# Optimization experiments

Hardware: AMD Instinct MI355X
Metric: run time of the kernel (lower is better)

## Reference

```python
import jax, jax.numpy as jnp
import numpy as np

EPS = 1e-5

def inorm(x, w, b):
    # InstanceNorm1d over token dim (axis=1), per (batch, feature); biased var
    m = x.mean(axis=1, keepdims=True)
    v = ((x - m) ** 2).mean(axis=1, keepdims=True)
    return (x - m) / jnp.sqrt(v + EPS) * w + b

def setup_inputs() -> dict:
    B, N, D, FH = 2, 512, 128, 512
    key = jax.random.key(0)
    ks = iter(jax.random.split(key, 48))
    rn = lambda shape, s=0.05: jax.random.normal(next(ks), shape, jnp.float32) * s
    inp = {
        'row_emb': jax.random.normal(next(ks), (B, N, D), jnp.float32),
        'col_emb': jax.random.normal(next(ks), (B, N, D), jnp.float32),
        'cost_mat': jax.random.uniform(next(ks), (B, N, N), jnp.float32),
        'coords': jax.random.uniform(next(ks), (B, N, 2), jnp.float32),
        'alpha': jnp.ones((1,), jnp.float32),
        # instance norm affine params (weight~1, bias~0)
        'n1_w': 1.0 + rn((D,)), 'n1_b': rn((D,)),
        'n2_w': 1.0 + rn((D,)), 'n2_b': rn((D,)),
        'n3_w': 1.0 + rn((D,)), 'n3_b': rn((D,)),
        'fn1_w': 1.0 + rn((D,)), 'fn1_b': rn((D,)),
        'fn2_w': 1.0 + rn((D,)), 'fn2_b': rn((D,)),
        # AFTFull projections (stored (in,out))
        'q_w': rn((D, D)), 'q_b': rn((D,)),
        'k_w': rn((D, D)), 'k_b': rn((D,)),
        'v_w': rn((D, D)), 'v_b': rn((D,)),
        'p_w': rn((D, D)), 'p_b': rn((D,)),
        'mhc_w': rn((D, D)), 'mhc_b': rn((D,)),
        # DistAngleFusion MLPs
        'dist_w1': rn((1, D)), 'dist_b1': rn((D,)),
        'dist_w2': rn((D, D)), 'dist_b2': rn((D,)),
        'ang_w1': rn((1, D)), 'ang_b1': rn((D,)),
        'ang_w2': rn((D, D)), 'ang_b2': rn((D,)),
        'gate_w': rn((2 * D, 1)), 'gate_b': rn((1,)),
        'outlin_w': rn((D, 1)), 'outlin_b': rn((1,)),
        # FeedForward
        'ffn_w1': rn((D, FH)), 'ffn_b1': rn((FH,)),
        'ffn_w2': rn((FH, D)), 'ffn_b2': rn((D,)),
    }
    return inp

def reference(row_emb, col_emb, cost_mat, coords, alpha,
              n1_w, n1_b, n2_w, n2_b, n3_w, n3_b, fn1_w, fn1_b, fn2_w, fn2_b,
              q_w, q_b, k_w, k_b, v_w, v_b, p_w, p_b, mhc_w, mhc_b,
              dist_w1, dist_b1, dist_w2, dist_b2,
              ang_w1, ang_b1, ang_w2, ang_b2,
              gate_w, gate_b, outlin_w, outlin_b,
              ffn_w1, ffn_b1, ffn_w2, ffn_b2):
    rn = inorm(row_emb, n1_w, n1_b)
    cn = inorm(col_emb, n2_w, n2_b)

    # DistAngleFusion: adapt_bias (B,N,N)
    diff = coords[:, :, None, :] - coords[:, None, :, :]  # (B,N,N,2)
    angles = jnp.arctan2(diff[..., 1], diff[..., 0])
    dist_e = jax.nn.relu(cost_mat[..., None] @ dist_w1 + dist_b1) @ dist_w2 + dist_b2  # (B,N,N,D)
    angle_e = jax.nn.relu(angles[..., None] @ ang_w1 + ang_b1) @ ang_w2 + ang_b2
    g = jax.nn.sigmoid(jnp.concatenate([dist_e, angle_e], axis=-1) @ gate_w + gate_b)  # (B,N,N,1)
    fused = g * dist_e + (1.0 - g) * angle_e
    adapt_bias = (fused @ outlin_w + outlin_b)[..., 0] * alpha  # (B,N,N)

    # AFTFull
    Q = jax.nn.sigmoid(rn @ q_w + q_b)          # (B,N,H)
    K = jax.nn.softmax(cn @ k_w + k_b, axis=1)  # softmax over tokens
    V = cn @ v_w + v_b
    eab = jnp.exp(jax.nn.softmax(adapt_bias, axis=-1))  # (B,N,N)
    eK = jnp.exp(K)
    num = jnp.einsum('bnm,bmh->bnh', eab, eK * V)
    den = jnp.einsum('bnm,bmh->bnh', eab, eK)
    Yt = (Q * (num / den)) @ p_w + p_b

    mh = inorm(Yt @ mhc_w + mhc_b, n3_w, n3_b)

    # TransformerFFN with instance norms
    x = inorm(rn + mh, fn1_w, fn1_b)
    ff = jax.nn.relu(x @ ffn_w1 + ffn_b1) @ ffn_w2 + ffn_b2
    return inorm(x + ff, fn2_w, fn2_b)
```

## Files before the change

kernel.cpp:

```cpp
#include <hip/hip_runtime.h>
#include <hip/hip_bf16.h>
#include <math.h>

#define Bn  2
#define Nn  512
#define Dn  128
#define FHn 512
#define BND (Bn*Nn*Dn)

typedef __hip_bfloat16 bf16;

__device__ __forceinline__ float cvt(float x) { return x; }
__device__ __forceinline__ float cvt(bf16 x) { return __bfloat162float(x); }
__device__ __forceinline__ float sigmoidf_(float x) { return 1.0f / (1.0f + expf(-x)); }
__device__ __forceinline__ bool is_bf16(const void* alpha) {
    return ((const unsigned short*)alpha)[0] == 0x3F80;
}

#define S_ 131072
#define WS_Q    (0 * S_)
#define WS_K    (1 * S_)
#define WS_V    (2 * S_)
#define WS_EK   (3 * S_)
#define WS_EKV  (4 * S_)
#define WS_EAB  (5 * S_)
#define WS_MH   (1 * S_)
#define WS_T    (2 * S_)
#define WS_OP   (3 * S_)
#define WS_ST   (9 * S_)

#define ST_IN_SC   0
#define ST_IN_SH   512
#define ST_X_SC    2048
#define ST_X_SH    2304
#define ST_PRE     3072
#define P_SC       1024
#define ST_TAB     4224

#define TAB_ANG 644
#define TAB_N   1288

#define SMEM_FLOATS 2568

struct KP {
    const void *row, *col, *cost, *coords, *alpha;
    const void *n1w, *n1b, *n2w, *n2b, *n3w, *n3b, *f1w, *f1b, *f2w, *f2b;
    const void *qw, *qb, *kw, *kb, *vw, *vb, *pw, *pb, *mw, *mb;
    const void *dw1, *db1, *dw2, *db2, *aw1, *ab1, *aw2, *ab2, *gw, *gb, *ow, *ob;
    const void *ffw1, *ffb1, *ffw2, *ffb2;
    void* out;
    float* ws;
};

__device__ __forceinline__ void blk_sum2(float& s, float& ss, volatile float* scr) {
#pragma unroll
    for (int off = 32; off > 0; off >>= 1) { s += __shfl_down(s, off); ss += __shfl_down(ss, off); }
    __syncthreads();
    int wave = threadIdx.x >> 6, lane = threadIdx.x & 63;
    if (lane == 0) { scr[wave] = s; scr[4 + wave] = ss; }
    __syncthreads();
    s = scr[0] + scr[1] + scr[2] + scr[3];
    ss = scr[4] + scr[5] + scr[6] + scr[7];
}

__device__ __forceinline__ float blk_sum1(float v, volatile float* scr) {
#pragma unroll
    for (int off = 32; off > 0; off >>= 1) v += __shfl_down(v, off);
    __syncthreads();
    int wave = threadIdx.x >> 6, lane = threadIdx.x & 63;
    if (lane == 0) scr[wave] = v;
    __syncthreads();
    return scr[0] + scr[1] + scr[2] + scr[3];
}

__device__ __forceinline__ float blk_max1(float v, volatile float* scr) {
#pragma unroll
    for (int off = 32; off > 0; off >>= 1) v = fmaxf(v, __shfl_down(v, off));
    __syncthreads();
    int wave = threadIdx.x >> 6, lane = threadIdx.x & 63;
    if (lane == 0) scr[wave] = v;
    __syncthreads();
    return fmaxf(fmaxf(scr[0], scr[1]), fmaxf(scr[2], scr[3]));
}

template <typename T>
__device__ void build_tables(const T* w1p, const T* b1p, const T* w2p,
                             const T* owp, const T* gwp, float* gtab, float* smem) {
    int tid = threadIdx.x;
    float* W  = smem;
    float* Bb = smem + 128;
    float* U  = smem + 256;
    float* Vv = smem + 384;
    float* Tt = smem + 512;
    int* RK   = (int*)(smem + 640);
    if (tid < 128) {
        float u = 0.f, v = 0.f;
#pragma unroll 4
        for (int d = 0; d < Dn; ++d) {
            float w2 = cvt(w2p[tid * Dn + d]);
            u += w2 * cvt(owp[d]);
            v += w2 * cvt(gwp[d]);
        }
        float w = cvt(w1p[tid]), b = cvt(b1p[tid]);
        U[tid] = u; Vv[tid] = v; W[tid] = w; Bb[tid] = b;
        Tt[tid] = (w != 0.f) ? (-b / w) : 3.0e38f;
    }
    __syncthreads();
    if (tid < 128) {
        float tk = Tt[tid]; int r = 0;
        for (int j = 0; j < 128; ++j) {
            float tj = Tt[j];
            r += (tj < tk) || (tj == tk && j < tid);
        }
        RK[tid] = r;
        gtab[r] = tk;
    }
    __syncthreads();
    if (tid <= 128) {
        int si = tid;
        float slS = 0, inS = 0, slT = 0, inT = 0;
        for (int k = 0; k < 128; ++k) {
            float w = W[k];
            if (w == 0.f) {
                float rb = fmaxf(Bb[k], 0.f);
                inS += rb * U[k];
                inT += rb * Vv[k];
            } else {
                bool act = (w > 0.f) ? (RK[k] < si) : (RK[k] >= si);
                if (act) {
                    slS += w * U[k];  inS += Bb[k] * U[k];
                    slT += w * Vv[k]; inT += Bb[k] * Vv[k];
                }
            }
        }
        gtab[128 + si] = slS;
        gtab[257 + si] = inS;
        gtab[386 + si] = slT;
        gtab[515 + si] = inT;
    }
}

__device__ __forceinline__ int bsearch128(const float* T, float c) {
    int lo = 0, hi = 128;
    while (lo < hi) { int mid = (lo + hi) >> 1; if (T[mid] <= c) lo = mid + 1; else hi = mid; }
    return lo;
}

template <typename T>
__device__ void phase0(const KP& p, float* st, float* smem) {
    float* scr = smem + 2560;
    int cid = blockIdx.x;
    int tid = threadIdx.x;
    {
        int which = cid >> 8, b = (cid >> 7) & 1, d = cid & 127;
        const T* src = (const T*)(which ? p.col : p.row) + (size_t)b * Nn * Dn + d;
        float x0 = cvt(src[(size_t)tid * Dn]);
        float x1 = cvt(src[(size_t)(tid + 256) * Dn]);
        float s = x0 + x1, ss = x0 * x0 + x1 * x1;
        blk_sum2(s, ss, scr);
        if (tid == 0) {
            float m = s * (1.f / Nn);
            float v = fmaxf(ss * (1.f / Nn) - m * m, 0.f);
            float rstd = rsqrtf(v + 1e-5f);
            const T* w = which ? (const T*)p.n2w : (const T*)p.n1w;
            const T* bb = which ? (const T*)p.n2b : (const T*)p.n1b;
            float sc = rstd * cvt(w[d]);
            st[ST_IN_SC + cid] = sc;
            st[ST_IN_SH + cid] = cvt(bb[d]) - m * sc;
        }
    }
    __syncthreads();
    if (cid == 128) {
        const T* db2 = (const T*)p.db2; const T* ab2 = (const T*)p.ab2;
        const T* ow = (const T*)p.ow;   const T* gw = (const T*)p.gw;
        float d2 = 0.f, a2 = 0.f, o = 0.f, g0 = 0.f, g1 = 0.f;
        if (tid < 128) {
            d2 = cvt(db2[tid]); a2 = cvt(ab2[tid]);
            o = cvt(ow[tid]); g0 = cvt(gw[tid]); g1 = cvt(gw[Dn + tid]);
        }
        float cds = d2 * o, cdt = d2 * g0, cas = a2 * o, cat = a2 * g1;
        blk_sum2(cds, cdt, scr);
        blk_sum2(cas, cat, scr);
        if (tid == 0) {
            float* pre = st + ST_PRE;
            pre[P_SC + 0] = cds; pre[P_SC + 1] = cdt;
            pre[P_SC + 2] = cas; pre[P_SC + 3] = cat;
            pre[P_SC + 4] = cvt(((const T*)p.gb)[0]);
            pre[P_SC + 5] = cvt(((const T*)p.ob)[0]);
            pre[P_SC + 6] = cvt(((const T*)p.alpha)[0]);
        }
    } else if (cid == 129) {
        build_tables<T>((const T*)p.dw1, (const T*)p.db1, (const T*)p.dw2,
                        (const T*)p.ow, (const T*)p.gw, st + ST_TAB, smem);
    } else if (cid == 130) {
        build_tables<T>((const T*)p.aw1, (const T*)p.ab1, (const T*)p.aw2,
                        (const T*)p.ow, (const T*)p.gw + Dn, st + ST_TAB + TAB_ANG, smem);
    }
}

template <typename T>
__device__ void phase1(const KP& p, float* st, float* smem) {
    int tid = threadIdx.x;
    int r0 = blockIdx.x * 2;
    int b = r0 >> 9;
    const T* row = (const T*)p.row; const T* col = (const T*)p.col;
    float* ws = p.ws;
    float* Q = ws + WS_Q; float* Kraw = ws + WS_K; float* V = ws + WS_V;

    float* lr = smem;
    float* lc = smem + 256;
    float* redq = smem + 512;
    float* redk = smem + 1024;
    float* redv = smem + 1536;
    {
        int r = tid >> 7, d = tid & 127;
        float scR = st[ST_IN_SC + b * 128 + d],       shR = st[ST_IN_SH + b * 128 + d];
        float scC = st[ST_IN_SC + 256 + b * 128 + d], shC = st[ST_IN_SH + 256 + b * 128 + d];
        lr[r * 128 + d] = cvt(row[(size_t)(r0 + r) * Dn + d]) * scR + shR;
        lc[r * 128 + d] = cvt(col[(size_t)(r0 + r) * Dn + d]) * scC + shC;
    }
    __syncthreads();
    {
        int h = tid & 127, half = tid >> 7;
        const T* qw = (const T*)p.qw; const T* kw = (const T*)p.kw; const T* vw = (const T*)p.vw;
        float q0 = 0, q1 = 0, ka = 0, kb_ = 0, v0 = 0, v1 = 0;
        int ks = half * 64;
#pragma unroll 8
        for (int k = ks; k < ks + 64; ++k) {
            float wq = cvt(qw[k * Dn + h]);
            float wk = cvt(kw[k * Dn + h]);
            float wv = cvt(vw[k * Dn + h]);
            q0 += lr[k] * wq;        q1 += lr[128 + k] * wq;
            ka += lc[k] * wk;        kb_ += lc[128 + k] * wk;
            v0 += lc[k] * wv;        v1 += lc[128 + k] * wv;
        }
        redq[half * 256 + h] = q0;  redq[half * 256 + 128 + h] = q1;
        redk[half * 256 + h] = ka;  redk[half * 256 + 128 + h] = kb_;
        redv[half * 256 + h] = v0;  redv[half * 256 + 128 + h] = v1;
    }
    __syncthreads();
    if (tid < 128) {
        int h = tid;
        float bq = cvt(((const T*)p.qb)[h]);
        float bk = cvt(((const T*)p.kb)[h]);
        float bv = cvt(((const T*)p.vb)[h]);
#pragma unroll
        for (int r = 0; r < 2; ++r) {
            Q[(r0 + r) * Dn + h]    = sigmoidf_(redq[r * 128 + h] + redq[256 + r * 128 + h] + bq);
            Kraw[(r0 + r) * Dn + h] = redk[r * 128 + h] + redk[256 + r * 128 + h] + bk;
            V[(r0 + r) * Dn + h]    = redv[r * 128 + h] + redv[256 + r * 128 + h] + bv;
        }
    }
    __syncthreads();

    float* abv = smem;
    float* red = smem + 512;
    float* tab = smem + 768;
    const float* gtab = st + ST_TAB;
    for (int e = tid; e < TAB_N; e += 256) tab[e] = gtab[e];
    __syncthreads();
    float* eab = ws + WS_EAB;
    const float* pre = st + ST_PRE;
    float cds = pre[P_SC + 0], cdt = pre[P_SC + 1], cas = pre[P_SC + 2], cat = pre[P_SC + 3];
    float gbias = pre[P_SC + 4], obias = pre[P_SC + 5], alpha = pre[P_SC + 6];
    const T* cost = (const T*)p.cost;
    const T* coords = (const T*)p.coords;

    for (int rr = 0; rr < 2; ++rr) {
        int rowi = r0 + rr;
        int bb_ = rowi >> 9, i = rowi & 511;
        float cix = cvt(coords[((size_t)bb_ * Nn + i) * 2 + 0]);
        float ciy = cvt(coords[((size_t)bb_ * Nn + i) * 2 + 1]);
        const T* crow = cost + (size_t)bb_ * Nn * Nn + (size_t)i * Nn;
#pragma unroll
        for (int jj = 0; jj < 2; ++jj) {
            int j = tid + jj * 256;
            float c = cvt(crow[j]);
            int si = bsearch128(tab, c);
            float sd = fmaf(tab[128 + si], c, tab[257 + si]) + cds;
            float td = fmaf(tab[386 + si], c, tab[515 + si]) + cdt;
            float dx = cix - cvt(coords[((size_t)bb_ * Nn + j) * 2 + 0]);
            float dy = ciy - cvt(coords[((size_t)bb_ * Nn + j) * 2 + 1]);
            float ang = (dx == 0.f && dy == 0.f) ? 0.f : atan2f(dy, dx);
            int ai = bsearch128(tab + TAB_ANG, ang);
            float sa = fmaf(tab[TAB_ANG + 128 + ai], ang, tab[TAB_ANG + 257 + ai]) + cas;
            float ta = fmaf(tab[TAB_ANG + 386 + ai], ang, tab[TAB_ANG + 515 + ai]) + cat;
            float gv = sigmoidf_(td + ta + gbias);
            abv[j] = alpha * (gv * sd + (1.f - gv) * sa + obias);
        }
        __syncthreads();
        float m = fmaxf(abv[tid], abv[tid + 256]);
        red[tid] = m; __syncthreads();
        for (int s = 128; s > 0; s >>= 1) {
            if (tid < s) red[tid] = fmaxf(red[tid], red[tid + s]);
            __syncthreads();
        }
        m = red[0];
        __syncthreads();
        float e0 = expf(abv[tid] - m), e1 = expf(abv[tid + 256] - m);
        red[tid] = e0 + e1; __syncthreads();
        for (int s = 128; s > 0; s >>= 1) {
            if (tid < s) red[tid] += red[tid + s];
            __syncthreads();
        }
        float rsum = 1.f / red[0];
        float* orow = eab + (size_t)rowi * Nn;
        orow[tid] = expf(e0 * rsum);
        orow[tid + 256] = expf(e1 * rsum);
        __syncthreads();
    }
}

__device__ void phase2(const KP& p, float* smem) {
    float* scr = smem + 2560;
    int tid = threadIdx.x;
    int c = blockIdx.x;
    int b = c >> 7, h = c & 127;
    float* ws = p.ws;
    const float* Kraw = ws + WS_K;
    const float* V = ws + WS_V;
    float* eK = ws + WS_EK;
    float* eKV = ws + WS_EKV;
    const float* kb = Kraw + (size_t)b * Nn * Dn + h;
    const float* vb = V + (size_t)b * Nn * Dn + h;
    float x0 = kb[(size_t)tid * Dn];
    float x1 = kb[(size_t)(tid + 256) * Dn];
    float mx = blk_max1(fmaxf(x0, x1), scr);
    float e0 = expf(x0 - mx), e1 = expf(x1 - mx);
    float s = blk_sum1(e0 + e1, scr);
    float rs = 1.f / s;
    size_t a0 = (size_t)b * Nn * Dn + (size_t)tid * Dn + h;
    size_t a1 = (size_t)b * Nn * Dn + (size_t)(tid + 256) * Dn + h;
    float ek0 = expf(e0 * rs), ek1 = expf(e1 * rs);
    eK[a0] = ek0;  eKV[a0] = ek0 * vb[(size_t)tid * Dn];
    eK[a1] = ek1;  eKV[a1] = ek1 * vb[(size_t)(tid + 256) * Dn];
}

template <typename T>
__device__ void phase3(const KP& p, float* smem) {
    int tid = threadIdx.x;
    int r0 = blockIdx.x * 4;
    int b = r0 >> 9;
    float* ws = p.ws;
    const float* eab = ws + WS_EAB;
    const float* eK = ws + WS_EK;
    const float* eKV = ws + WS_EKV;
    const float* Q = ws + WS_Q;
    float* mh = ws + WS_MH;

    float* ab   = smem;
    float* redn = smem + 2048;
    float* redd = smem + 4096;
    float* gl   = smem + 6144;
    float* yl   = smem + 6656;

    {
        float4* ab4 = (float4*)ab;
        const float4* g4 = (const float4*)(eab + (size_t)r0 * Nn);
        ab4[tid] = g4[tid];
    }
    __syncthreads();
    int h = tid & 127, q = tid >> 7;
    {
        float num[4] = {0,0,0,0}, den[4] = {0,0,0,0};
        int j0 = q * 128;
        const float* ekb = eK + (size_t)b * Nn * Dn + h;
        const float* evb = eKV + (size_t)b * Nn * Dn + h;
#pragma unroll 4
        for (int j = j0; j < j0 + 128; ++j) {
            float ek = ekb[(size_t)j * Dn];
            float ev = evb[(size_t)j * Dn];
#pragma unroll
            for (int r = 0; r < 4; ++r) {
                num[r] += ab[r * 512 + j] * ev;
                den[r] += ab[r * 512 + j] * ek;
            }
        }
#pragma unroll
        for (int r = 0; r < 4; ++r) {
            redn[q * 512 + r * 128 + h] = num[r];
            redd[q * 512 + r * 128 + h] = den[r];
        }
    }
    __syncthreads();
    if (tid < 128) {
#pragma unroll
        for (int r = 0; r < 4; ++r) {
            float nu = redn[r * 128 + h] + redn[512 + r * 128 + h]
                     + redn[1024 + r * 128 + h] + redn[1536 + r * 128 + h];
            float de = redd[r * 128 + h] + redd[512 + r * 128 + h]
                     + redd[1024 + r * 128 + h] + redd[1536 + r * 128 + h];
            gl[r * 128 + h] = Q[(r0 + r) * Dn + h] * nu / de;
        }
    }
    __syncthreads();
    {
        const T* pw = (const T*)p.pw;
        float acc[4] = {0,0,0,0};
        int ks = q * 32;
#pragma unroll 8
        for (int k = ks; k < ks + 32; ++k) {
            float w = cvt(pw[k * Dn + h]);
#pragma unroll
            for (int r = 0; r < 4; ++r) acc[r] += gl[r * 128 + k] * w;
        }
#pragma unroll
        for (int r = 0; r < 4; ++r) redn[q * 512 + r * 128 + h] = acc[r];
    }
    __syncthreads();
    if (tid < 128) {
        float bp = cvt(((const T*)p.pb)[h]);
#pragma unroll
        for (int r = 0; r < 4; ++r)
            yl[r * 128 + h] = redn[r * 128 + h] + redn[512 + r * 128 + h]
                            + redn[1024 + r * 128 + h] + redn[1536 + r * 128 + h] + bp;
    }
    __syncthreads();
    {
        const T* mw = (const T*)p.mw;
        float acc[4] = {0,0,0,0};
        int ks = q * 32;
#pragma unroll 8
        for (int k = ks; k < ks + 32; ++k) {
            float w = cvt(mw[k * Dn + h]);
#pragma unroll
            for (int r = 0; r < 4; ++r) acc[r] += yl[r * 128 + k] * w;
        }
#pragma unroll
        for (int r = 0; r < 4; ++r) redn[q * 512 + r * 128 + h] = acc[r];
    }
    __syncthreads();
    if (tid < 128) {
        float bm = cvt(((const T*)p.mb)[h]);
#pragma unroll
        for (int r = 0; r < 4; ++r)
            mh[(r0 + r) * Dn + h] = redn[r * 128 + h] + redn[512 + r * 128 + h]
                                  + redn[1024 + r * 128 + h] + redn[1536 + r * 128 + h] + bm;
    }
}

template <typename T>
__device__ void phase45(const KP& p, float* st, float* smem) {
    float* scr = smem + 2560;
    int tid = threadIdx.x;
    int c = blockIdx.x;
    int b = c >> 7, d = c & 127;
    const float* mh = p.ws + WS_MH;
    const float* mp = mh + (size_t)b * Nn * Dn + d;
    float m0 = mp[(size_t)tid * Dn], m1 = mp[(size_t)(tid + 256) * Dn];
    float s = m0 + m1, ss = m0 * m0 + m1 * m1;
    blk_sum2(s, ss, scr);
    float mm = s * (1.f / Nn);
    float vv = fmaxf(ss * (1.f / Nn) - mm * mm, 0.f);
    float rstd = rsqrtf(vv + 1e-5f);
    float scM = rstd * cvt(((const T*)p.n3w)[d]);
    float shM = cvt(((const T*)p.n3b)[d]) - mm * scM;
    const T* row = (const T*)p.row;
    float scI = st[ST_IN_SC + c], shI = st[ST_IN_SH + c];
    const T* rp = row + (size_t)b * Nn * Dn + d;
    float* tp = p.ws + WS_T + (size_t)b * Nn * Dn + d;
    float x0 = cvt(rp[(size_t)tid * Dn]) * scI + shI + m0 * scM + shM;
    float x1 = cvt(rp[(size_t)(tid + 256) * Dn]) * scI + shI + m1 * scM + shM;
    tp[(size_t)tid * Dn] = x0;
    tp[(size_t)(tid + 256) * Dn] = x1;
    __syncthreads();
    float s2 = x0 + x1, ss2 = x0 * x0 + x1 * x1;
    blk_sum2(s2, ss2, scr);
    if (tid == 0) {
        float m = s2 * (1.f / Nn);
        float v = fmaxf(ss2 * (1.f / Nn) - m * m, 0.f);
        float r = rsqrtf(v + 1e-5f);
        float sc = r * cvt(((const T*)p.f1w)[d]);
        st[ST_X_SC + c] = sc;
        st[ST_X_SH + c] = cvt(((const T*)p.f1b)[d]) - m * sc;
    }
}

template <typename T>
__device__ void phase6(const KP& p, float* st, float* smem) {
    int tid = threadIdx.x;
    int r0 = blockIdx.x * 4;
    int b = r0 >> 9;
    const float* t = p.ws + WS_T;
    float* outpre = p.ws + WS_OP;
    const T* w1 = (const T*)p.ffw1; const T* b1 = (const T*)p.ffb1;
    const T* w2 = (const T*)p.ffw2; const T* b2 = (const T*)p.ffb2;

    float* xl = smem;
    float* hl = smem + 512;
    float* red = smem + 2560;
    {
        int r = tid >> 7, d = tid & 127;
        int c = b * 128 + d;
        xl[r * 128 + d] = t[(r0 + r) * Dn + d] * st[ST_X_SC + c] + st[ST_X_SH + c];
    }
    __syncthreads();
    {
        int f = tid;
        float a[4] = {0,0,0,0};
#pragma unroll 4
        for (int k = 0; k < Dn; ++k) {
            float w = cvt(w1[k * FHn + f]);
#pragma unroll
            for (int r = 0; r < 4; ++r) a[r] += xl[r * 128 + k] * w;
        }
        float bb1 = cvt(b1[f]);
#pragma unroll
        for (int r = 0; r < 4; ++r) hl[r * 512 + f] = fmaxf(a[r] + bb1, 0.f);
    }
    __syncthreads();
    {
        int d = tid & 127, q = tid >> 7;
        int k0 = q * 128;
        float a[4] = {0,0,0,0};
#pragma unroll 8
        for (int k = k0; k < k0 + 128; ++k) {
            float w = cvt(w2[k * Dn + d]);
#pragma unroll
            for (int r = 0; r < 4; ++r) a[r] += hl[r * 512 + k] * w;
        }
#pragma unroll
        for (int r = 0; r < 4; ++r) red[q * 512 + r * 128 + d] = a[r];
    }
    __syncthreads();
    if (tid < 128) {
        float bb2 = cvt(b2[tid]);
#pragma unroll
        for (int r = 0; r < 4; ++r) {
            float sum = red[r * 128 + tid] + red[512 + r * 128 + tid]
                      + red[1024 + r * 128 + tid] + red[1536 + r * 128 + tid];
            outpre[(r0 + r) * Dn + tid] = xl[r * 128 + tid] + sum + bb2;
        }
    }
}

template <typename T>
__device__ void phase78(const KP& p, float* smem) {
    float* scr = smem + 2560;
    int tid = threadIdx.x;
    int c = blockIdx.x;
    int b = c >> 7, d = c & 127;
    const float* op = p.ws + WS_OP;
    const float* sp = op + (size_t)b * Nn * Dn + d;
    float x0 = sp[(size_t)tid * Dn], x1 = sp[(size_t)(tid + 256) * Dn];
    float s = x0 + x1, ss = x0 * x0 + x1 * x1;
    blk_sum2(s, ss, scr);
    float m = s * (1.f / Nn);
    float v = fmaxf(ss * (1.f / Nn) - m * m, 0.f);
    float rstd = rsqrtf(v + 1e-5f);
    float sc = rstd * cvt(((const T*)p.f2w)[d]);
    float sh = cvt(((const T*)p.f2b)[d]) - m * sc;
    T* out = (T*)p.out + (size_t)b * Nn * Dn + d;
    out[(size_t)tid * Dn] = (T)(x0 * sc + sh);
    out[(size_t)(tid + 256) * Dn] = (T)(x1 * sc + sh);
}

#define PH_WRAP(name, call_bf, call_f)                                        \
__global__ __launch_bounds__(256) void name(KP p) {                           \
    __shared__ float smem[SMEM_FLOATS];                                       \
    float* st = p.ws + WS_ST; (void)st;                                       \
    if (is_bf16(p.alpha)) { call_bf; } else { call_f; }                       \
}

PH_WRAP(k_head,  phase0<bf16>(p, st, smem),  phase0<float>(p, st, smem))
PH_WRAP(k_qkveab, phase1<bf16>(p, st, smem), phase1<float>(p, st, smem))
__global__ __launch_bounds__(256) void k_kekv(KP p) {
    __shared__ float smem[SMEM_FLOATS];
    phase2(p, smem);
}
__global__ __launch_bounds__(512) void k_attn(KP p) {
    __shared__ float smem[7168];
    if (is_bf16(p.alpha)) phase3<bf16>(p, smem);
    else                  phase3<float>(p, smem);
}
PH_WRAP(k_mid,   phase45<bf16>(p, st, smem), phase45<float>(p, st, smem))
__global__ __launch_bounds__(512) void k_ffn(KP p) {
    __shared__ float smem[4608];
    float* st = p.ws + WS_ST;
    if (is_bf16(p.alpha)) phase6<bf16>(p, st, smem);
    else                  phase6<float>(p, st, smem);
}
PH_WRAP(k_tail,  phase78<bf16>(p, smem),     phase78<float>(p, smem))

extern "C" void kernel_launch(void* const* d_in, const int* in_sizes, int n_in,
                              void* d_out, int out_size, void* d_ws, size_t ws_size,
                              hipStream_t stream) {
    KP p;
    p.row = d_in[0];  p.col = d_in[1];  p.cost = d_in[2];  p.coords = d_in[3];
    p.alpha = d_in[4];
    p.n1w = d_in[5];  p.n1b = d_in[6];  p.n2w = d_in[7];  p.n2b = d_in[8];
    p.n3w = d_in[9];  p.n3b = d_in[10]; p.f1w = d_in[11]; p.f1b = d_in[12];
    p.f2w = d_in[13]; p.f2b = d_in[14];
    p.qw = d_in[15];  p.qb = d_in[16];  p.kw = d_in[17];  p.kb = d_in[18];
    p.vw = d_in[19];  p.vb = d_in[20];  p.pw = d_in[21];  p.pb = d_in[22];
    p.mw = d_in[23];  p.mb = d_in[24];
    p.dw1 = d_in[25]; p.db1 = d_in[26]; p.dw2 = d_in[27]; p.db2 = d_in[28];
    p.aw1 = d_in[29]; p.ab1 = d_in[30]; p.aw2 = d_in[31]; p.ab2 = d_in[32];
    p.gw = d_in[33];  p.gb = d_in[34];  p.ow = d_in[35];  p.ob = d_in[36];
    p.ffw1 = d_in[37]; p.ffb1 = d_in[38]; p.ffw2 = d_in[39]; p.ffb2 = d_in[40];
    p.out = d_out;
    p.ws = (float*)d_ws;

    k_head<<<512, 256, 0, stream>>>(p);
    k_qkveab<<<512, 256, 0, stream>>>(p);
    k_kekv<<<256, 256, 0, stream>>>(p);
    k_attn<<<256, 512, 0, stream>>>(p);
    k_mid<<<256, 256, 0, stream>>>(p);
    k_ffn<<<256, 512, 0, stream>>>(p);
    k_tail<<<256, 256, 0, stream>>>(p);
}
```

Baseline: 240.8 us.

## Fuse seven phase kernels into one cooperative kernel with grid syncs

After: 435.6 us. 1.81x slower.

```diff
diff --git a/kernel.cpp b/kernel.cpp
--- a/kernel.cpp
+++ b/kernel.cpp
@@ -1,12 +1,14 @@
 #include <hip/hip_runtime.h>
 #include <hip/hip_bf16.h>
+#include <hip/hip_cooperative_groups.h>
 #include <math.h>
+
+namespace cg = cooperative_groups;
 
 #define Bn  2
 #define Nn  512
 #define Dn  128
 #define FHn 512
-#define BND (Bn*Nn*Dn)
 
 typedef __hip_bfloat16 bf16;
 
@@ -40,7 +42,7 @@
 #define TAB_ANG 644
 #define TAB_N   1288
 
-#define SMEM_FLOATS 2568
+#define SMEM_FLOATS 7232
 
 struct KP {
     const void *row, *col, *cost, *coords, *alpha;
@@ -52,35 +54,55 @@
     float* ws;
 };
 
-__device__ __forceinline__ void blk_sum2(float& s, float& ss, volatile float* scr) {
+__device__ __forceinline__ void blk512_sum2(float& s, float& ss, volatile float* scr) {
 #pragma unroll
     for (int off = 32; off > 0; off >>= 1) { s += __shfl_down(s, off); ss += __shfl_down(ss, off); }
     __syncthreads();
     int wave = threadIdx.x >> 6, lane = threadIdx.x & 63;
-    if (lane == 0) { scr[wave] = s; scr[4 + wave] = ss; }
-    __syncthreads();
-    s = scr[0] + scr[1] + scr[2] + scr[3];
-    ss = scr[4] + scr[5] + scr[6] + scr[7];
-}
-
-__device__ __forceinline__ float blk_sum1(float v, volatile float* scr) {
+    if (lane == 0) { scr[wave] = s; scr[8 + wave] = ss; }
+    __syncthreads();
+    s = 0.f; ss = 0.f;
+#pragma unroll
+    for (int w = 0; w < 8; ++w) { s += scr[w]; ss += scr[8 + w]; }
+}
+
+__device__ __forceinline__ float blk512_sum1(float v, volatile float* scr) {
 #pragma unroll
     for (int off = 32; off > 0; off >>= 1) v += __shfl_down(v, off);
     __syncthreads();
     int wave = threadIdx.x >> 6, lane = threadIdx.x & 63;
     if (lane == 0) scr[wave] = v;
     __syncthreads();
-    return scr[0] + scr[1] + scr[2] + scr[3];
-}
-
-__device__ __forceinline__ float blk_max1(float v, volatile float* scr) {
+    float s = 0.f;
+#pragma unroll
+    for (int w = 0; w < 8; ++w) s += scr[w];
+    return s;
+}
+
+__device__ __forceinline__ float blk512_max1(float v, volatile float* scr) {
 #pragma unroll
     for (int off = 32; off > 0; off >>= 1) v = fmaxf(v, __shfl_down(v, off));
     __syncthreads();
     int wave = threadIdx.x >> 6, lane = threadIdx.x & 63;
     if (lane == 0) scr[wave] = v;
     __syncthreads();
-    return fmaxf(fmaxf(scr[0], scr[1]), fmaxf(scr[2], scr[3]));
+    float m = scr[0];
+#pragma unroll
+    for (int w = 1; w < 8; ++w) m = fmaxf(m, scr[w]);
+    return m;
+}
+
+__device__ __forceinline__ void grp_sum2(float& s, float& ss, volatile float* scr) {
+#pragma unroll
+    for (int off = 32; off > 0; off >>= 1) { s += __shfl_down(s, off); ss += __shfl_down(ss, off); }
+    __syncthreads();
+    int tid = threadIdx.x;
+    int wave = tid >> 6, lane = tid & 63;
+    if (lane == 0) { scr[wave] = s; scr[8 + wave] = ss; }
+    __syncthreads();
+    int base = (tid >> 8) * 4;
+    s  = scr[base] + scr[base + 1] + scr[base + 2] + scr[base + 3];
+    ss = scr[8 + base] + scr[8 + base + 1] + scr[8 + base + 2] + scr[8 + base + 3];
 }
 
 template <typename T>
@@ -147,30 +169,32 @@
 }
 
 template <typename T>
-__device__ void phase0(const KP& p, float* st, float* smem) {
-    float* scr = smem + 2560;
-    int cid = blockIdx.x;
-    int tid = threadIdx.x;
-    {
-        int which = cid >> 8, b = (cid >> 7) & 1, d = cid & 127;
-        const T* src = (const T*)(which ? p.col : p.row) + (size_t)b * Nn * Dn + d;
-        float x0 = cvt(src[(size_t)tid * Dn]);
-        float x1 = cvt(src[(size_t)(tid + 256) * Dn]);
+__device__ void phase0_f(const KP& p, float* st, float* smem) {
+    float* scr = smem + 7168;
+    int tid = threadIdx.x;
+    int bid = blockIdx.x;
+    int g = tid >> 8, t = tid & 255;
+    int cid = bid + g * 256;
+    {
+        int b = (bid >> 7) & 1, d = bid & 127;
+        const T* src = (const T*)(g ? p.col : p.row) + (size_t)b * Nn * Dn + d;
+        float x0 = cvt(src[(size_t)t * Dn]);
+        float x1 = cvt(src[(size_t)(t + 256) * Dn]);
         float s = x0 + x1, ss = x0 * x0 + x1 * x1;
-        blk_sum2(s, ss, scr);
-        if (tid == 0) {
+        grp_sum2(s, ss, scr);
+        if (t == 0) {
             float m = s * (1.f / Nn);
             float v = fmaxf(ss * (1.f / Nn) - m * m, 0.f);
             float rstd = rsqrtf(v + 1e-5f);
-            const T* w = which ? (const T*)p.n2w : (const T*)p.n1w;
-            const T* bb = which ? (const T*)p.n2b : (const T*)p.n1b;
+            const T* w = g ? (const T*)p.n2w : (const T*)p.n1w;
+            const T* bb = g ? (const T*)p.n2b : (const T*)p.n1b;
             float sc = rstd * cvt(w[d]);
             st[ST_IN_SC + cid] = sc;
             st[ST_IN_SH + cid] = cvt(bb[d]) - m * sc;
         }
     }
     __syncthreads();
-    if (cid == 128) {
+    if (bid == 128) {
         const T* db2 = (const T*)p.db2; const T* ab2 = (const T*)p.ab2;
         const T* ow = (const T*)p.ow;   const T* gw = (const T*)p.gw;
         float d2 = 0.f, a2 = 0.f, o = 0.f, g0 = 0.f, g1 = 0.f;
@@ -179,8 +203,8 @@
             o = cvt(ow[tid]); g0 = cvt(gw[tid]); g1 = cvt(gw[Dn + tid]);
         }
         float cds = d2 * o, cdt = d2 * g0, cas = a2 * o, cat = a2 * g1;
-        blk_sum2(cds, cdt, scr);
-        blk_sum2(cas, cat, scr);
+        blk512_sum2(cds, cdt, scr);
+        blk512_sum2(cas, cat, scr);
         if (tid == 0) {
             float* pre = st + ST_PRE;
             pre[P_SC + 0] = cds; pre[P_SC + 1] = cdt;
@@ -189,29 +213,30 @@
             pre[P_SC + 5] = cvt(((const T*)p.ob)[0]);
             pre[P_SC + 6] = cvt(((const T*)p.alpha)[0]);
         }
-    } else if (cid == 129) {
+    } else if (bid == 129) {
         build_tables<T>((const T*)p.dw1, (const T*)p.db1, (const T*)p.dw2,
                         (const T*)p.ow, (const T*)p.gw, st + ST_TAB, smem);
-    } else if (cid == 130) {
+    } else if (bid == 130) {
         build_tables<T>((const T*)p.aw1, (const T*)p.ab1, (const T*)p.aw2,
                         (const T*)p.ow, (const T*)p.gw + Dn, st + ST_TAB + TAB_ANG, smem);
     }
 }
 
 template <typename T>
-__device__ void phase1(const KP& p, float* st, float* smem) {
-    int tid = threadIdx.x;
-    int r0 = blockIdx.x * 2;
+__device__ void phase1_f(const KP& p, float* st, float* smem) {
+    int tid = threadIdx.x;
+    int r0 = blockIdx.x * 4;
     int b = r0 >> 9;
     const T* row = (const T*)p.row; const T* col = (const T*)p.col;
     float* ws = p.ws;
     float* Q = ws + WS_Q; float* Kraw = ws + WS_K; float* V = ws + WS_V;
+    float* scr = smem + 7168;
 
     float* lr = smem;
-    float* lc = smem + 256;
-    float* redq = smem + 512;
-    float* redk = smem + 1024;
-    float* redv = smem + 1536;
+    float* lc = smem + 512;
+    float* redq = smem + 1024;
+    float* redk = smem + 3072;
+    float* redv = smem + 5120;
     {
         int r = tid >> 7, d = tid & 127;
         float scR = st[ST_IN_SC + b * 128 + d],       shR = st[ST_IN_SH + b * 128 + d];
@@ -221,22 +246,28 @@
     }
     __syncthreads();
     {
-        int h = tid & 127, half = tid >> 7;
+        int h = tid & 127, q = tid >> 7;
         const T* qw = (const T*)p.qw; const T* kw = (const T*)p.kw; const T* vw = (const T*)p.vw;
-        float q0 = 0, q1 = 0, ka = 0, kb_ = 0, v0 = 0, v1 = 0;
-        int ks = half * 64;
+        float aq[4] = {0,0,0,0}, ak[4] = {0,0,0,0}, av[4] = {0,0,0,0};
+        int ks = q * 32;
 #pragma unroll 8
-        for (int k = ks; k < ks + 64; ++k) {
+        for (int k = ks; k < ks + 32; ++k) {
             float wq = cvt(qw[k * Dn + h]);
             float wk = cvt(kw[k * Dn + h]);
             float wv = cvt(vw[k * Dn + h]);
-            q0 += lr[k] * wq;        q1 += lr[128 + k] * wq;
-            ka += lc[k] * wk;        kb_ += lc[128 + k] * wk;
-            v0 += lc[k] * wv;        v1 += lc[128 + k] * wv;
-        }
-        redq[half * 256 + h] = q0;  redq[half * 256 + 128 + h] = q1;
-        redk[half * 256 + h] = ka;  redk[half * 256 + 128 + h] = kb_;
-        redv[half * 256 + h] = v0;  redv[half * 256 + 128 + h] = v1;
+#pragma unroll
+            for (int r = 0; r < 4; ++r) {
+                aq[r] += lr[r * 128 + k] * wq;
+                ak[r] += lc[r * 128 + k] * wk;
+                av[r] += lc[r * 128 + k] * wv;
+            }
+        }
+#pragma unroll
+        for (int r = 0; r < 4; ++r) {
+            redq[q * 512 + r * 128 + h] = aq[r];
+            redk[q * 512 + r * 128 + h] = ak[r];
+            redv[q * 512 + r * 128 + h] = av[r];
+        }
     }
     __syncthreads();
     if (tid < 128) {
@@ -245,19 +276,20 @@
         float bk = cvt(((const T*)p.kb)[h]);
         float bv = cvt(((const T*)p.vb)[h]);
 #pragma unroll
-        for (int r = 0; r < 2; ++r) {
-            Q[(r0 + r) * Dn + h]    = sigmoidf_(redq[r * 128 + h] + redq[256 + r * 128 + h] + bq);
-            Kraw[(r0 + r) * Dn + h] = redk[r * 128 + h] + redk[256 + r * 128 + h] + bk;
-            V[(r0 + r) * Dn + h]    = redv[r * 128 + h] + redv[256 + r * 128 + h] + bv;
-        }
-    }
-    __syncthreads();
-
-    float* abv = smem;
-    float* red = smem + 512;
-    float* tab = smem + 768;
+        for (int r = 0; r < 4; ++r) {
+            float qv = redq[r*128+h] + redq[512 + r*128+h] + redq[1024 + r*128+h] + redq[1536 + r*128+h] + bq;
+            float kv = redk[r*128+h] + redk[512 + r*128+h] + redk[1024 + r*128+h] + redk[1536 + r*128+h] + bk;
+            float vv = redv[r*128+h] + redv[512 + r*128+h] + redv[1024 + r*128+h] + redv[1536 + r*128+h] + bv;
+            Q[(r0 + r) * Dn + h]    = sigmoidf_(qv);
+            Kraw[(r0 + r) * Dn + h] = kv;
+            V[(r0 + r) * Dn + h]    = vv;
+        }
+    }
+    __syncthreads();
+
+    float* tab = smem;
     const float* gtab = st + ST_TAB;
-    for (int e = tid; e < TAB_N; e += 256) tab[e] = gtab[e];
+    for (int e = tid; e < TAB_N; e += 512) tab[e] = gtab[e];
     __syncthreads();
     float* eab = ws + WS_EAB;
     const float* pre = st + ST_PRE;
@@ -266,53 +298,80 @@
     const T* cost = (const T*)p.cost;
     const T* coords = (const T*)p.coords;
 
-    for (int rr = 0; rr < 2; ++rr) {
+    int j = tid;
+    float aval[4];
+#pragma unroll
+    for (int rr = 0; rr < 4; ++rr) {
         int rowi = r0 + rr;
         int bb_ = rowi >> 9, i = rowi & 511;
         float cix = cvt(coords[((size_t)bb_ * Nn + i) * 2 + 0]);
         float ciy = cvt(coords[((size_t)bb_ * Nn + i) * 2 + 1]);
-        const T* crow = cost + (size_t)bb_ * Nn * Nn + (size_t)i * Nn;
-#pragma unroll
-        for (int jj = 0; jj < 2; ++jj) {
-            int j = tid + jj * 256;
-            float c = cvt(crow[j]);
-            int si = bsearch128(tab, c);
-            float sd = fmaf(tab[128 + si], c, tab[257 + si]) + cds;
-            float td = fmaf(tab[386 + si], c, tab[515 + si]) + cdt;
-            float dx = cix - cvt(coords[((size_t)bb_ * Nn + j) * 2 + 0]);
-            float dy = ciy - cvt(coords[((size_t)bb_ * Nn + j) * 2 + 1]);
-            float ang = (dx == 0.f && dy == 0.f) ? 0.f : atan2f(dy, dx);
-            int ai = bsearch128(tab + TAB_ANG, ang);
-            float sa = fmaf(tab[TAB_ANG + 128 + ai], ang, tab[TAB_ANG + 257 + ai]) + cas;
-            float ta = fmaf(tab[TAB_ANG + 386 + ai], ang, tab[TAB_ANG + 515 + ai]) + cat;
-            float gv = sigmoidf_(td + ta + gbias);
-            abv[j] = alpha * (gv * sd + (1.f - gv) * sa + obias);
+        float c = cvt(cost[(size_t)bb_ * Nn * Nn + (size_t)i * Nn + j]);
+        int si = bsearch128(tab, c);
+        float sd = fmaf(tab[128 + si], c, tab[257 + si]) + cds;
+        float td = fmaf(tab[386 + si], c, tab[515 + si]) + cdt;
+        float dx = cix - cvt(coords[((size_t)bb_ * Nn + j) * 2 + 0]);
+        float dy = ciy - cvt(coords[((size_t)bb_ * Nn + j) * 2 + 1]);
+        float ang = (dx == 0.f && dy == 0.f) ? 0.f : atan2f(dy, dx);
+        int ai = bsearch128(tab + TAB_ANG, ang);
+        float sa = fmaf(tab[TAB_ANG + 128 + ai], ang, tab[TAB_ANG + 257 + ai]) + cas;
+        float ta = fmaf(tab[TAB_ANG + 386 + ai], ang, tab[TAB_ANG + 515 + ai]) + cat;
+        float gv = sigmoidf_(td + ta + gbias);
+        aval[rr] = alpha * (gv * sd + (1.f - gv) * sa + obias);
+    }
+    int wave = tid >> 6, lane = tid & 63;
+    float mx[4];
+    {
+        float t0 = aval[0], t1 = aval[1], t2 = aval[2], t3 = aval[3];
+#pragma unroll
+        for (int off = 32; off > 0; off >>= 1) {
+            t0 = fmaxf(t0, __shfl_down(t0, off));
+            t1 = fmaxf(t1, __shfl_down(t1, off));
+            t2 = fmaxf(t2, __shfl_down(t2, off));
+            t3 = fmaxf(t3, __shfl_down(t3, off));
         }
         __syncthreads();
-        float m = fmaxf(abv[tid], abv[tid + 256]);
-        red[tid] = m; __syncthreads();
-        for (int s = 128; s > 0; s >>= 1) {
-            if (tid < s) red[tid] = fmaxf(red[tid], red[tid + s]);
-            __syncthreads();
-        }
-        m = red[0];
+        if (lane == 0) { scr[wave] = t0; scr[8 + wave] = t1; scr[16 + wave] = t2; scr[24 + wave] = t3; }
         __syncthreads();
-        float e0 = expf(abv[tid] - m), e1 = expf(abv[tid + 256] - m);
-        red[tid] = e0 + e1; __syncthreads();
-        for (int s = 128; s > 0; s >>= 1) {
-            if (tid < s) red[tid] += red[tid + s];
-            __syncthreads();
-        }
-        float rsum = 1.f / red[0];
-        float* orow = eab + (size_t)rowi * Nn;
-        orow[tid] = expf(e0 * rsum);
-        orow[tid + 256] = expf(e1 * rsum);
+#pragma unroll
+        for (int rr = 0; rr < 4; ++rr) {
+            float m = scr[rr * 8];
+#pragma unroll
+            for (int w = 1; w < 8; ++w) m = fmaxf(m, scr[rr * 8 + w]);
+            mx[rr] = m;
+        }
+    }
+    float ev[4];
+#pragma unroll
+    for (int rr = 0; rr < 4; ++rr) ev[rr] = expf(aval[rr] - mx[rr]);
+    float rs[4];
+    {
+        float t0 = ev[0], t1 = ev[1], t2 = ev[2], t3 = ev[3];
+#pragma unroll
+        for (int off = 32; off > 0; off >>= 1) {
+            t0 += __shfl_down(t0, off);
+            t1 += __shfl_down(t1, off);
+            t2 += __shfl_down(t2, off);
+            t3 += __shfl_down(t3, off);
+        }
         __syncthreads();
-    }
-}
-
-__device__ void phase2(const KP& p, float* smem) {
-    float* scr = smem + 2560;
+        if (lane == 0) { scr[wave] = t0; scr[8 + wave] = t1; scr[16 + wave] = t2; scr[24 + wave] = t3; }
+        __syncthreads();
+#pragma unroll
+        for (int rr = 0; rr < 4; ++rr) {
+            float s = 0.f;
+#pragma unroll
+            for (int w = 0; w < 8; ++w) s += scr[rr * 8 + w];
+            rs[rr] = 1.f / s;
+        }
+    }
+#pragma unroll
+    for (int rr = 0; rr < 4; ++rr)
+        eab[(size_t)(r0 + rr) * Nn + j] = expf(ev[rr] * rs[rr]);
+}
+
+__device__ void phase2_f(const KP& p, float* smem) {
+    float* scr = smem + 7168;
     int tid = threadIdx.x;
     int c = blockIdx.x;
     int b = c >> 7, h = c & 127;
@@ -324,20 +383,17 @@
     const float* kb = Kraw + (size_t)b * Nn * Dn + h;
     const float* vb = V + (size_t)b * Nn * Dn + h;
     float x0 = kb[(size_t)tid * Dn];
-    float x1 = kb[(size_t)(tid + 256) * Dn];
-    float mx = blk_max1(fmaxf(x0, x1), scr);
-    float e0 = expf(x0 - mx), e1 = expf(x1 - mx);
-    float s = blk_sum1(e0 + e1, scr);
-    float rs = 1.f / s;
+    float mx = blk512_max1(x0, scr);
+    float e0 = expf(x0 - mx);
+    float s = blk512_sum1(e0, scr);
+    float rsv = 1.f / s;
     size_t a0 = (size_t)b * Nn * Dn + (size_t)tid * Dn + h;
-    size_t a1 = (size_t)b * Nn * Dn + (size_t)(tid + 256) * Dn + h;
-    float ek0 = expf(e0 * rs), ek1 = expf(e1 * rs);
+    float ek0 = expf(e0 * rsv);
     eK[a0] = ek0;  eKV[a0] = ek0 * vb[(size_t)tid * Dn];
-    eK[a1] = ek1;  eKV[a1] = ek1 * vb[(size_t)(tid + 256) * Dn];
-}
-
-template <typename T>
-__device__ void phase3(const KP& p, float* smem) {
+}
+
+template <typename T>
+__device__ void phase3_f(const KP& p, float* smem) {
     int tid = threadIdx.x;
     int r0 = blockIdx.x * 4;
     int b = r0 >> 9;
@@ -367,13 +423,13 @@
         const float* ekb = eK + (size_t)b * Nn * Dn + h;
         const float* evb = eKV + (size_t)b * Nn * Dn + h;
 #pragma unroll 4
-        for (int j = j0; j < j0 + 128; ++j) {
-            float ek = ekb[(size_t)j * Dn];
-            float ev = evb[(size_t)j * Dn];
+        for (int jj = j0; jj < j0 + 128; ++jj) {
+            float ek = ekb[(size_t)jj * Dn];
+            float ev = evb[(size_t)jj * Dn];
 #pragma unroll
             for (int r = 0; r < 4; ++r) {
-                num[r] += ab[r * 512 + j] * ev;
-                den[r] += ab[r * 512 + j] * ek;
+                num[r] += ab[r * 512 + jj] * ev;
+                den[r] += ab[r * 512 + jj] * ek;
             }
         }
 #pragma unroll
@@ -440,16 +496,16 @@
 }
 
 template <typename T>
-__device__ void phase45(const KP& p, float* st, float* smem) {
-    float* scr = smem + 2560;
+__device__ void phase45_f(const KP& p, float* st, float* smem) {
+    float* scr = smem + 7168;
     int tid = threadIdx.x;
     int c = blockIdx.x;
     int b = c >> 7, d = c & 127;
     const float* mh = p.ws + WS_MH;
     const float* mp = mh + (size_t)b * Nn * Dn + d;
-    float m0 = mp[(size_t)tid * Dn], m1 = mp[(size_t)(tid + 256) * Dn];
-    float s = m0 + m1, ss = m0 * m0 + m1 * m1;
-    blk_sum2(s, ss, scr);
+    float m0 = mp[(size_t)tid * Dn];
+    float s = m0, ss = m0 * m0;
+    blk512_sum2(s, ss, scr);
     float mm = s * (1.f / Nn);
     float vv = fmaxf(ss * (1.f / Nn) - mm * mm, 0.f);
     float rstd = rsqrtf(vv + 1e-5f);
@@ -460,12 +516,9 @@
     const T* rp = row + (size_t)b * Nn * Dn + d;
     float* tp = p.ws + WS_T + (size_t)b * Nn * Dn + d;
     float x0 = cvt(rp[(size_t)tid * Dn]) * scI + shI + m0 * scM + shM;
-    float x1 = cvt(rp[(size_t)(tid + 256) * Dn]) * scI + shI + m1 * scM + shM;
     tp[(size_t)tid * Dn] = x0;
-    tp[(size_t)(tid + 256) * Dn] = x1;
-    __syncthreads();
-    float s2 = x0 + x1, ss2 = x0 * x0 + x1 * x1;
-    blk_sum2(s2, ss2, scr);
+    float s2 = x0, ss2 = x0 * x0;
+    blk512_sum2(s2, ss2, scr);
     if (tid == 0) {
         float m = s2 * (1.f / Nn);
         float v = fmaxf(ss2 * (1.f / Nn) - m * m, 0.f);
@@ -477,7 +530,7 @@
 }
 
 template <typename T>
-__device__ void phase6(const KP& p, float* st, float* smem) {
+__device__ void phase6_f(const KP& p, float* st, float* smem) {
     int tid = threadIdx.x;
     int r0 = blockIdx.x * 4;
     int b = r0 >> 9;
@@ -535,16 +588,16 @@
 }
 
 template <typename T>
-__device__ void phase78(const KP& p, float* smem) {
-    float* scr = smem + 2560;
+__device__ void phase78_f(const KP& p, float* smem) {
+    float* scr = smem + 7168;
     int tid = threadIdx.x;
     int c = blockIdx.x;
     int b = c >> 7, d = c & 127;
     const float* op = p.ws + WS_OP;
     const float* sp = op + (size_t)b * Nn * Dn + d;
-    float x0 = sp[(size_t)tid * Dn], x1 = sp[(size_t)(tid + 256) * Dn];
-    float s = x0 + x1, ss = x0 * x0 + x1 * x1;
-    blk_sum2(s, ss, scr);
+    float x0 = sp[(size_t)tid * Dn];
+    float s = x0, ss = x0 * x0;
+    blk512_sum2(s, ss, scr);
     float m = s * (1.f / Nn);
     float v = fmaxf(ss * (1.f / Nn) - m * m, 0.f);
     float rstd = rsqrtf(v + 1e-5f);
@@ -552,35 +605,32 @@
     float sh = cvt(((const T*)p.f2b)[d]) - m * sc;
     T* out = (T*)p.out + (size_t)b * Nn * Dn + d;
     out[(size_t)tid * Dn] = (T)(x0 * sc + sh);
-    out[(size_t)(tid + 256) * Dn] = (T)(x1 * sc + sh);
-}
-
-#define PH_WRAP(name, call_bf, call_f)                                        \
-__global__ __launch_bounds__(256) void name(KP p) {                           \
-    __shared__ float smem[SMEM_FLOATS];                                       \
-    float* st = p.ws + WS_ST; (void)st;                                       \
-    if (is_bf16(p.alpha)) { call_bf; } else { call_f; }                       \
-}
-
-PH_WRAP(k_head,  phase0<bf16>(p, st, smem),  phase0<float>(p, st, smem))
-PH_WRAP(k_qkveab, phase1<bf16>(p, st, smem), phase1<float>(p, st, smem))
-__global__ __launch_bounds__(256) void k_kekv(KP p) {
+}
+
+template <typename T>
+__device__ void run_all(const KP& p, float* smem, cg::grid_group& grid) {
+    float* st = p.ws + WS_ST;
+    phase0_f<T>(p, st, smem);
+    grid.sync();
+    phase1_f<T>(p, st, smem);
+    grid.sync();
+    phase2_f(p, smem);
+    grid.sync();
+    phase3_f<T>(p, smem);
+    grid.sync();
+    phase45_f<T>(p, st, smem);
+    grid.sync();
+    phase6_f<T>(p, st, smem);
+    grid.sync();
+    phase78_f<T>(p, smem);
+}
+
+__global__ __launch_bounds__(512, 1) void k_all(KP p) {
     __shared__ float smem[SMEM_FLOATS];
-    phase2(p, smem);
-}
-__global__ __launch_bounds__(512) void k_attn(KP p) {
-    __shared__ float smem[7168];
-    if (is_bf16(p.alpha)) phase3<bf16>(p, smem);
-    else                  phase3<float>(p, smem);
-}
-PH_WRAP(k_mid,   phase45<bf16>(p, st, smem), phase45<float>(p, st, smem))
-__global__ __launch_bounds__(512) void k_ffn(KP p) {
-    __shared__ float smem[4608];
-    float* st = p.ws + WS_ST;
-    if (is_bf16(p.alpha)) phase6<bf16>(p, st, smem);
-    else                  phase6<float>(p, st, smem);
-}
-PH_WRAP(k_tail,  phase78<bf16>(p, smem),     phase78<float>(p, smem))
+    cg::grid_group grid = cg::this_grid();
+    if (is_bf16(p.alpha)) run_all<bf16>(p, smem, grid);
+    else                  run_all<float>(p, smem, grid);
+}
 
 extern "C" void kernel_launch(void* const* d_in, const int* in_sizes, int n_in,
                               void* d_out, int out_size, void* d_ws, size_t ws_size,
@@ -601,11 +651,6 @@
     p.out = d_out;
     p.ws = (float*)d_ws;
 
-    k_head<<<512, 256, 0, stream>>>(p);
-    k_qkveab<<<512, 256, 0, stream>>>(p);
-    k_kekv<<<256, 256, 0, stream>>>(p);
-    k_attn<<<256, 512, 0, stream>>>(p);
-    k_mid<<<256, 256, 0, stream>>>(p);
-    k_ffn<<<256, 512, 0, stream>>>(p);
-    k_tail<<<256, 256, 0, stream>>>(p);
-}
+    void* args[] = { (void*)&p };
+    hipLaunchCooperativeKernel((void*)k_all, dim3(256), dim3(512), args, 0u, stream);
+}
```

## Replace bsearch with LUT-bucketed search, fast atan2/exp, and warp-level softmax reductions

Applied to the files above, without the earlier changes.

After: 241.4 us. No clear change (+0.2%).

```diff
diff --git a/kernel.cpp b/kernel.cpp
--- a/kernel.cpp
+++ b/kernel.cpp
@@ -6,15 +6,29 @@
 #define Nn  512
 #define Dn  128
 #define FHn 512
-#define BND (Bn*Nn*Dn)
+
+#define PI_F 3.14159265358979323846f
 
 typedef __hip_bfloat16 bf16;
 
 __device__ __forceinline__ float cvt(float x) { return x; }
 __device__ __forceinline__ float cvt(bf16 x) { return __bfloat162float(x); }
-__device__ __forceinline__ float sigmoidf_(float x) { return 1.0f / (1.0f + expf(-x)); }
+__device__ __forceinline__ float sigmoidf_(float x) { return 1.0f / (1.0f + __expf(-x)); }
 __device__ __forceinline__ bool is_bf16(const void* alpha) {
     return ((const unsigned short*)alpha)[0] == 0x3F80;
+}
+
+__device__ __forceinline__ float fatan2f(float dy, float dx) {
+    float ax = fabsf(dx), ay = fabsf(dy);
+    float mx = fmaxf(ax, ay), mn = fminf(ax, ay);
+    float r = __fdividef(mn, mx);
+    float t = r * r;
+    float a = r * (0.99997726f + t * (-0.33262347f + t * (0.19354346f +
+              t * (-0.11643287f + t * (0.05265332f + t * (-0.01172120f))))));
+    if (ay > ax) a = 1.57079632679489662f - a;
+    if (dx < 0.f) a = PI_F - a;
+    if (dy < 0.f) a = -a;
+    return fminf(fmaxf(a, -PI_F), PI_F);
 }
 
 #define S_ 131072
@@ -36,9 +50,11 @@
 #define ST_PRE     3072
 #define P_SC       1024
 #define ST_TAB     4224
-
 #define TAB_ANG 644
 #define TAB_N   1288
+#define ST_LUTC (ST_TAB + TAB_N)
+#define ST_LUTA (ST_LUTC + 257)
+#define TABLUT_N (TAB_N + 514)
 
 #define SMEM_FLOATS 2568
 
@@ -93,6 +109,7 @@
     float* Vv = smem + 384;
     float* Tt = smem + 512;
     int* RK   = (int*)(smem + 640);
+    float* STl = smem + 768;
     if (tid < 128) {
         float u = 0.f, v = 0.f;
 #pragma unroll 4
@@ -114,6 +131,7 @@
         }
         RK[tid] = r;
         gtab[r] = tk;
+        STl[r] = tk;
     }
     __syncthreads();
     if (tid <= 128) {
@@ -192,9 +210,21 @@
     } else if (cid == 129) {
         build_tables<T>((const T*)p.dw1, (const T*)p.db1, (const T*)p.dw2,
                         (const T*)p.ow, (const T*)p.gw, st + ST_TAB, smem);
+        __syncthreads();
+        const float* STl = smem + 768;
+        for (int e = tid; e < 257; e += 256) {
+            float c = e * (1.f / 256.f);
+            st[ST_LUTC + e] = (float)bsearch128(STl, c);
+        }
     } else if (cid == 130) {
         build_tables<T>((const T*)p.aw1, (const T*)p.ab1, (const T*)p.aw2,
                         (const T*)p.ow, (const T*)p.gw + Dn, st + ST_TAB + TAB_ANG, smem);
+        __syncthreads();
+        const float* STl = smem + 768;
+        for (int e = tid; e < 257; e += 256) {
+            float a = -PI_F + e * (PI_F / 128.f);
+            st[ST_LUTA + e] = (float)bsearch128(STl, a);
+        }
     }
 }
 
@@ -253,11 +283,12 @@
     }
     __syncthreads();
 
-    float* abv = smem;
-    float* red = smem + 512;
-    float* tab = smem + 768;
-    const float* gtab = st + ST_TAB;
-    for (int e = tid; e < TAB_N; e += 256) tab[e] = gtab[e];
+    float* tab  = smem;
+    float* lutc = smem + 1288;
+    float* luta = smem + 1545;
+    float* scr  = smem + 1824;
+    const float* gt = st + ST_TAB;
+    for (int e = tid; e < TABLUT_N; e += 256) smem[e] = gt[e];
     __syncthreads();
     float* eab = ws + WS_EAB;
     const float* pre = st + ST_PRE;
@@ -265,50 +296,65 @@
     float gbias = pre[P_SC + 4], obias = pre[P_SC + 5], alpha = pre[P_SC + 6];
     const T* cost = (const T*)p.cost;
     const T* coords = (const T*)p.coords;
-
+    const float* tabA = tab + TAB_ANG;
+
+    float av[2][2];
+#pragma unroll
     for (int rr = 0; rr < 2; ++rr) {
         int rowi = r0 + rr;
-        int bb_ = rowi >> 9, i = rowi & 511;
-        float cix = cvt(coords[((size_t)bb_ * Nn + i) * 2 + 0]);
-        float ciy = cvt(coords[((size_t)bb_ * Nn + i) * 2 + 1]);
-        const T* crow = cost + (size_t)bb_ * Nn * Nn + (size_t)i * Nn;
+        int i = rowi & 511;
+        float cix = cvt(coords[((size_t)b * Nn + i) * 2 + 0]);
+        float ciy = cvt(coords[((size_t)b * Nn + i) * 2 + 1]);
+        const T* crow = cost + (size_t)b * Nn * Nn + (size_t)i * Nn;
 #pragma unroll
         for (int jj = 0; jj < 2; ++jj) {
             int j = tid + jj * 256;
             float c = cvt(crow[j]);
-            int si = bsearch128(tab, c);
-            float sd = fmaf(tab[128 + si], c, tab[257 + si]) + cds;
-            float td = fmaf(tab[386 + si], c, tab[515 + si]) + cdt;
-            float dx = cix - cvt(coords[((size_t)bb_ * Nn + j) * 2 + 0]);
-            float dy = ciy - cvt(coords[((size_t)bb_ * Nn + j) * 2 + 1]);
-            float ang = (dx == 0.f && dy == 0.f) ? 0.f : atan2f(dy, dx);
-            int ai = bsearch128(tab + TAB_ANG, ang);
-            float sa = fmaf(tab[TAB_ANG + 128 + ai], ang, tab[TAB_ANG + 257 + ai]) + cas;
-            float ta = fmaf(tab[TAB_ANG + 386 + ai], ang, tab[TAB_ANG + 515 + ai]) + cat;
+            int k = (int)(c * 256.f); k = k < 0 ? 0 : (k > 255 ? 255 : k);
+            int lo = (int)lutc[k], hi = (int)lutc[k + 1];
+            while (lo < hi && tab[lo] <= c) ++lo;
+            float sd = fmaf(tab[128 + lo], c, tab[257 + lo]) + cds;
+            float td = fmaf(tab[386 + lo], c, tab[515 + lo]) + cdt;
+            float dx = cix - cvt(coords[((size_t)b * Nn + j) * 2 + 0]);
+            float dy = ciy - cvt(coords[((size_t)b * Nn + j) * 2 + 1]);
+            float ang = (dx == 0.f && dy == 0.f) ? 0.f : fatan2f(dy, dx);
+            int ka = (int)((ang + PI_F) * (128.f / PI_F)); ka = ka < 0 ? 0 : (ka > 255 ? 255 : ka);
+            int la = (int)luta[ka], ha = (int)luta[ka + 1];
+            while (la < ha && tabA[la] <= ang) ++la;
+            float sa = fmaf(tabA[128 + la], ang, tabA[257 + la]) + cas;
+            float ta = fmaf(tabA[386 + la], ang, tabA[515 + la]) + cat;
             float gv = sigmoidf_(td + ta + gbias);
-            abv[j] = alpha * (gv * sd + (1.f - gv) * sa + obias);
-        }
-        __syncthreads();
-        float m = fmaxf(abv[tid], abv[tid + 256]);
-        red[tid] = m; __syncthreads();
-        for (int s = 128; s > 0; s >>= 1) {
-            if (tid < s) red[tid] = fmaxf(red[tid], red[tid + s]);
-            __syncthreads();
-        }
-        m = red[0];
-        __syncthreads();
-        float e0 = expf(abv[tid] - m), e1 = expf(abv[tid + 256] - m);
-        red[tid] = e0 + e1; __syncthreads();
-        for (int s = 128; s > 0; s >>= 1) {
-            if (tid < s) red[tid] += red[tid + s];
-            __syncthreads();
-        }
-        float rsum = 1.f / red[0];
-        float* orow = eab + (size_t)rowi * Nn;
-        orow[tid] = expf(e0 * rsum);
-        orow[tid + 256] = expf(e1 * rsum);
-        __syncthreads();
-    }
+            av[rr][jj] = alpha * (gv * sd + (1.f - gv) * sa + obias);
+        }
+    }
+    int wave = tid >> 6, lane = tid & 63;
+    float m0 = fmaxf(av[0][0], av[0][1]);
+    float m1 = fmaxf(av[1][0], av[1][1]);
+#pragma unroll
+    for (int off = 32; off > 0; off >>= 1) {
+        m0 = fmaxf(m0, __shfl_down(m0, off));
+        m1 = fmaxf(m1, __shfl_down(m1, off));
+    }
+    if (lane == 0) { scr[wave] = m0; scr[4 + wave] = m1; }
+    __syncthreads();
+    float mx0 = fmaxf(fmaxf(scr[0], scr[1]), fmaxf(scr[2], scr[3]));
+    float mx1 = fmaxf(fmaxf(scr[4], scr[5]), fmaxf(scr[6], scr[7]));
+    float e00 = __expf(av[0][0] - mx0), e01 = __expf(av[0][1] - mx0);
+    float e10 = __expf(av[1][0] - mx1), e11 = __expf(av[1][1] - mx1);
+    float s0 = e00 + e01, s1 = e10 + e11;
+#pragma unroll
+    for (int off = 32; off > 0; off >>= 1) {
+        s0 += __shfl_down(s0, off);
+        s1 += __shfl_down(s1, off);
+    }
+    if (lane == 0) { scr[8 + wave] = s0; scr[12 + wave] = s1; }
+    __syncthreads();
+    float rs0 = 1.f / (scr[8] + scr[9] + scr[10] + scr[11]);
+    float rs1 = 1.f / (scr[12] + scr[13] + scr[14] + scr[15]);
+    float* o0 = eab + (size_t)r0 * Nn;
+    float* o1 = eab + (size_t)(r0 + 1) * Nn;
+    o0[tid] = __expf(e00 * rs0);  o0[tid + 256] = __expf(e01 * rs0);
+    o1[tid] = __expf(e10 * rs1);  o1[tid + 256] = __expf(e11 * rs1);
 }
 
 __device__ void phase2(const KP& p, float* smem) {
@@ -326,12 +372,12 @@
     float x0 = kb[(size_t)tid * Dn];
     float x1 = kb[(size_t)(tid + 256) * Dn];
     float mx = blk_max1(fmaxf(x0, x1), scr);
-    float e0 = expf(x0 - mx), e1 = expf(x1 - mx);
+    float e0 = __expf(x0 - mx), e1 = __expf(x1 - mx);
     float s = blk_sum1(e0 + e1, scr);
     float rs = 1.f / s;
     size_t a0 = (size_t)b * Nn * Dn + (size_t)tid * Dn + h;
     size_t a1 = (size_t)b * Nn * Dn + (size_t)(tid + 256) * Dn + h;
-    float ek0 = expf(e0 * rs), ek1 = expf(e1 * rs);
+    float ek0 = __expf(e0 * rs), ek1 = __expf(e1 * rs);
     eK[a0] = ek0;  eKV[a0] = ek0 * vb[(size_t)tid * Dn];
     eK[a1] = ek1;  eKV[a1] = ek1 * vb[(size_t)(tid + 256) * Dn];
 }
```
